# Kernel tuning notes

Measured on AMD Instinct MI355X. Metric: run time of the kernel, lower is better.

Reference implementation:

```python
import jax, jax.numpy as jnp
import numpy as np

B, NB, F, N = 8192, 64, 256, 1_000_000
K = 8            # per-channel top-k
KS = K // 2 + 1  # conv1d kernel size = 5
H, OUT = 256, 128
DN = ('NWC', 'WIO', 'NWC')


def setup_inputs() -> dict:
    key = jax.random.key(0)
    ks = jax.random.split(key, 7)
    return {
        'node_ids': jax.random.randint(ks[0], (B,), 0, N, dtype=jnp.int64) if jax.config.jax_enable_x64 else jax.random.randint(ks[0], (B,), 0, N, dtype=jnp.int32),
        'neighbors': jax.random.randint(ks[1], (B, NB), 0, N, dtype=jnp.int32),
        'feat_table': jax.random.normal(ks[2], (N, F), dtype=jnp.float32),
        'W1': jax.random.normal(ks[3], (KS, F, H), dtype=jnp.float32) * 0.05,
        'b1': jnp.zeros((H,), dtype=jnp.float32),
        'W2': jax.random.normal(ks[4], (KS, H, OUT), dtype=jnp.float32) * 0.05,
        'b2': jnp.zeros((OUT,), dtype=jnp.float32),
    }


def reference(node_ids, neighbors, feat_table, W1, b1, W2, b2):
    node_feats = feat_table[node_ids][:, None, :]          # [B, 1, F]
    nb_feats = feat_table[neighbors]                       # [B, NB, F] irregular gather
    # per-channel top-k over neighbors
    topk, _ = jax.lax.top_k(jnp.transpose(nb_feats, (0, 2, 1)), K)  # [B, F, K]
    topk = jnp.transpose(topk, (0, 2, 1))                  # [B, K, F]
    x = jnp.concatenate([node_feats, topk], axis=1)        # [B, K+1, F]
    h = jax.lax.conv_general_dilated(x, W1, (1,), 'VALID', dimension_numbers=DN) + b1  # [B, K+2-KS, H]
    o = jax.lax.conv_general_dilated(h, W2, (1,), 'VALID', dimension_numbers=DN) + b2  # [B, 1, OUT]
    return o[:, 0, :]                                      # [B, OUT]
```

## Files before the change

kernel.cpp:

```cpp
#include <hip/hip_runtime.h>
#include <hip/hip_bf16.h>

namespace {
constexpr int kB    = 8192;
constexpr int kNB   = 64;
constexpr int kF    = 256;
constexpr int kK    = 8;
constexpr int kKS   = 5;
constexpr int kH    = 256;
constexpr int kOUT  = 128;
constexpr int kXR   = 9;
constexpr int kTO   = 5;

constexpr size_t X_OFF   = 0;
constexpr size_t W1T_OFF = (size_t)kB * kXR * kF * 2;
constexpr size_t W2T_OFF = W1T_OFF + (size_t)kKS * kH * kF * 2;

typedef __attribute__((ext_vector_type(8))) short short8;
typedef __attribute__((ext_vector_type(4))) float f32x4;
}

using bf16 = __hip_bfloat16;

__device__ __forceinline__ unsigned short f2bf(float f) {
  bf16 h = __float2bfloat16(f);
  return *reinterpret_cast<unsigned short*>(&h);
}

__global__ void convert_weights(const float* __restrict__ W1,
                                const float* __restrict__ W2,
                                bf16* __restrict__ w1t, bf16* __restrict__ w2t)
{
  const int i = blockIdx.x * 256 + threadIdx.x;
  const int stride = gridDim.x * 256;
  for (int idx = i; idx < kKS * kH * kF; idx += stride) {
    const int f  = idx & 255;
    const int hc = (idx >> 8) & 255;
    const int dt = idx >> 16;
    w1t[idx] = __float2bfloat16(W1[(dt * kF + f) * kH + hc]);
  }
  for (int idx = i; idx < kOUT * kKS * kH; idx += stride) {
    const int k = idx % (kKS * kH);
    const int o = idx / (kKS * kH);
    w2t[idx] = __float2bfloat16(W2[k * kOUT + o]);
  }
}

__global__ __launch_bounds__(256)
void gather_topk(const int* __restrict__ node_ids,
                 const int* __restrict__ neighbors,
                 const float* __restrict__ feat,
                 bf16* __restrict__ x)
{
  const int wave = threadIdx.x >> 6;
  const int lane = threadIdx.x & 63;
  const int b    = blockIdx.x * 4 + wave;
  const int f4   = lane << 2;

  const int myn = neighbors[(size_t)b * kNB + lane];
  const int nid = node_ids[b];

  const float4 nodev =
      *reinterpret_cast<const float4*>(feat + (size_t)nid * kF + f4);

  float tk[4][kK];
#pragma unroll
  for (int c = 0; c < 4; ++c)
#pragma unroll
    for (int k = 0; k < kK; ++k) tk[c][k] = -INFINITY;

#pragma unroll 16
  for (int n = 0; n < kNB; ++n) {
    const int r = __builtin_amdgcn_readlane(myn, n);
    const float4 v =
        *reinterpret_cast<const float4*>(feat + (size_t)r * kF + f4);
    const float vv[4] = {v.x, v.y, v.z, v.w};
#pragma unroll
    for (int c = 0; c < 4; ++c) {
      tk[c][kK - 1] = fmaxf(tk[c][kK - 1], vv[c]);
#pragma unroll
      for (int k = kK - 1; k > 0; --k) {
        const float hi = fmaxf(tk[c][k - 1], tk[c][k]);
        const float lo = fminf(tk[c][k - 1], tk[c][k]);
        tk[c][k - 1] = hi;
        tk[c][k]     = lo;
      }
    }
  }

  bf16* xb = x + (size_t)b * kXR * kF + f4;
  {
    ushort4 s = {f2bf(nodev.x), f2bf(nodev.y), f2bf(nodev.z), f2bf(nodev.w)};
    *reinterpret_cast<ushort4*>(xb) = s;
  }
#pragma unroll
  for (int k = 0; k < kK; ++k) {
    ushort4 s = {f2bf(tk[0][k]), f2bf(tk[1][k]), f2bf(tk[2][k]), f2bf(tk[3][k])};
    *reinterpret_cast<ushort4*>(xb + (size_t)(1 + k) * kF) = s;
  }
}

__global__ __launch_bounds__(256)
void conv_gemm(const bf16* __restrict__ x, const bf16* __restrict__ w1t,
               const bf16* __restrict__ w2t, const float* __restrict__ b1,
               const float* __restrict__ b2, float* __restrict__ out)
{
  constexpr int BM   = 16;
  constexpr int XPAD = 264;
  constexpr int HPAD = 1288;

  __shared__ bf16 smem[BM * kXR * XPAD];
  bf16* xs = smem;
  bf16* hs = smem;

  const int tid  = threadIdx.x;
  const int wave = tid >> 6;
  const int lane = tid & 63;
  const int r = lane & 15;
  const int q = lane >> 4;
  const int bbase = blockIdx.x * BM;

  {
    const bf16* gx = x + (size_t)bbase * kXR * kF;
    for (int c = tid; c < BM * kXR * (kF / 8); c += 256) {
      const int f8  = c & 31;
      const int row = (c >> 5) % kXR;
      const int bb  = c / (32 * kXR);
      short8 v = *reinterpret_cast<const short8*>(gx + (size_t)c * 8);
      *reinterpret_cast<short8*>(&xs[(bb * kXR + row) * XPAD + f8 * 8]) = v;
    }
  }
  __syncthreads();

  const int ntb = wave * 64;
  f32x4 acc[kTO][4];
#pragma unroll
  for (int n = 0; n < 4; ++n) {
    const float bv = b1[ntb + n * 16 + r];
#pragma unroll
    for (int m = 0; m < kTO; ++m) acc[m][n] = (f32x4){bv, bv, bv, bv};
  }

  for (int kk = 0; kk < 8; ++kk) {
    short8 a[kXR];
#pragma unroll
    for (int rr = 0; rr < kXR; ++rr)
      a[rr] = *reinterpret_cast<const short8*>(&xs[(r * kXR + rr) * XPAD + kk * 32 + q * 8]);
#pragma unroll
    for (int dt = 0; dt < kKS; ++dt) {
      short8 bfr[4];
#pragma unroll
      for (int n = 0; n < 4; ++n)
        bfr[n] = *reinterpret_cast<const short8*>(
            &w1t[((size_t)(dt * kH + ntb + n * 16 + r)) * kF + kk * 32 + q * 8]);
#pragma unroll
      for (int m = 0; m < kTO; ++m)
#pragma unroll
        for (int n = 0; n < 4; ++n)
          acc[m][n] = __builtin_amdgcn_mfma_f32_16x16x32_bf16(a[m + dt], bfr[n], acc[m][n], 0, 0, 0);
    }
  }
  __syncthreads();

#pragma unroll
  for (int m = 0; m < kTO; ++m)
#pragma unroll
    for (int n = 0; n < 4; ++n)
#pragma unroll
      for (int j = 0; j < 4; ++j)
        hs[(q * 4 + j) * HPAD + m * kH + ntb + n * 16 + r] = __float2bfloat16(acc[m][n][j]);
  __syncthreads();

  const int ob = wave * 32;
  f32x4 acc2[2];
#pragma unroll
  for (int n = 0; n < 2; ++n) {
    const float bv = b2[ob + n * 16 + r];
    acc2[n] = (f32x4){bv, bv, bv, bv};
  }
  for (int ks = 0; ks < 40; ++ks) {
    short8 a2 = *reinterpret_cast<const short8*>(&hs[r * HPAD + ks * 32 + q * 8]);
#pragma unroll
    for (int n = 0; n < 2; ++n) {
      short8 b2f = *reinterpret_cast<const short8*>(
          &w2t[(size_t)(ob + n * 16 + r) * (kKS * kH) + ks * 32 + q * 8]);
      acc2[n] = __builtin_amdgcn_mfma_f32_16x16x32_bf16(a2, b2f, acc2[n], 0, 0, 0);
    }
  }
#pragma unroll
  for (int n = 0; n < 2; ++n)
#pragma unroll
    for (int j = 0; j < 4; ++j)
      out[(size_t)(bbase + q * 4 + j) * kOUT + ob + n * 16 + r] = acc2[n][j];
}

extern "C" void kernel_launch(void* const* d_in, const int* in_sizes, int n_in,
                              void* d_out, int out_size, void* d_ws, size_t ws_size,
                              hipStream_t stream) {
  const int*   node_ids  = (const int*)  d_in[0];
  const int*   neighbors = (const int*)  d_in[1];
  const float* feat      = (const float*)d_in[2];
  const float* W1        = (const float*)d_in[3];
  const float* b1        = (const float*)d_in[4];
  const float* W2        = (const float*)d_in[5];
  const float* b2        = (const float*)d_in[6];
  float* out = (float*)d_out;

  char* ws = (char*)d_ws;
  bf16* x_ws  = (bf16*)(ws + X_OFF);
  bf16* w1t   = (bf16*)(ws + W1T_OFF);
  bf16* w2t   = (bf16*)(ws + W2T_OFF);

  convert_weights<<<512, 256, 0, stream>>>(W1, W2, w1t, w2t);
  gather_topk<<<kB / 4, 256, 0, stream>>>(node_ids, neighbors, feat, x_ws);
  conv_gemm<<<kB / 16, 256, 0, stream>>>(x_ws, w1t, w2t, b1, b2, out);
}
```

Before: 168.6 us.

## Fuse neighbor gather and top-k into conv GEMM kernel with prefetch buffering

Merges the gather/top-k kernel into the conv GEMM kernel. Each wave computes top-k for four batch rows and writes the bf16 rows straight into LDS instead of a global workspace, which removes the intermediate x round trip and one launch. The neighbor row loads are now software-pipelined through an 8-deep register buffer to hide gather latency. The LDS padding changes to 258/1290 elements, which breaks 16-byte alignment of the vector LDS accesses, and each block now serializes gather work before its MFMA phase.

```diff
diff --git a/kernel.cpp b/kernel.cpp
--- a/kernel.cpp
+++ b/kernel.cpp
@@ -11,9 +11,12 @@
 constexpr int kOUT  = 128;
 constexpr int kXR   = 9;
 constexpr int kTO   = 5;
-
-constexpr size_t X_OFF   = 0;
-constexpr size_t W1T_OFF = (size_t)kB * kXR * kF * 2;
+constexpr int kBM   = 16;
+
+constexpr int XPAD = 258;
+constexpr int HPAD = 1290;
+
+constexpr size_t W1T_OFF = 0;
 constexpr size_t W2T_OFF = W1T_OFF + (size_t)kKS * kH * kF * 2;
 
 typedef __attribute__((ext_vector_type(8))) short short8;
@@ -47,69 +50,14 @@
 }
 
 __global__ __launch_bounds__(256)
-void gather_topk(const int* __restrict__ node_ids,
-                 const int* __restrict__ neighbors,
-                 const float* __restrict__ feat,
-                 bf16* __restrict__ x)
+void fused_all(const int* __restrict__ node_ids,
+               const int* __restrict__ neighbors,
+               const float* __restrict__ feat,
+               const bf16* __restrict__ w1t, const bf16* __restrict__ w2t,
+               const float* __restrict__ b1, const float* __restrict__ b2,
+               float* __restrict__ out)
 {
-  const int wave = threadIdx.x >> 6;
-  const int lane = threadIdx.x & 63;
-  const int b    = blockIdx.x * 4 + wave;
-  const int f4   = lane << 2;
-
-  const int myn = neighbors[(size_t)b * kNB + lane];
-  const int nid = node_ids[b];
-
-  const float4 nodev =
-      *reinterpret_cast<const float4*>(feat + (size_t)nid * kF + f4);
-
-  float tk[4][kK];
-#pragma unroll
-  for (int c = 0; c < 4; ++c)
-#pragma unroll
-    for (int k = 0; k < kK; ++k) tk[c][k] = -INFINITY;
-
-#pragma unroll 16
-  for (int n = 0; n < kNB; ++n) {
-    const int r = __builtin_amdgcn_readlane(myn, n);
-    const float4 v =
-        *reinterpret_cast<const float4*>(feat + (size_t)r * kF + f4);
-    const float vv[4] = {v.x, v.y, v.z, v.w};
-#pragma unroll
-    for (int c = 0; c < 4; ++c) {
-      tk[c][kK - 1] = fmaxf(tk[c][kK - 1], vv[c]);
-#pragma unroll
-      for (int k = kK - 1; k > 0; --k) {
-        const float hi = fmaxf(tk[c][k - 1], tk[c][k]);
-        const float lo = fminf(tk[c][k - 1], tk[c][k]);
-        tk[c][k - 1] = hi;
-        tk[c][k]     = lo;
-      }
-    }
-  }
-
-  bf16* xb = x + (size_t)b * kXR * kF + f4;
-  {
-    ushort4 s = {f2bf(nodev.x), f2bf(nodev.y), f2bf(nodev.z), f2bf(nodev.w)};
-    *reinterpret_cast<ushort4*>(xb) = s;
-  }
-#pragma unroll
-  for (int k = 0; k < kK; ++k) {
-    ushort4 s = {f2bf(tk[0][k]), f2bf(tk[1][k]), f2bf(tk[2][k]), f2bf(tk[3][k])};
-    *reinterpret_cast<ushort4*>(xb + (size_t)(1 + k) * kF) = s;
-  }
-}
-
-__global__ __launch_bounds__(256)
-void conv_gemm(const bf16* __restrict__ x, const bf16* __restrict__ w1t,
-               const bf16* __restrict__ w2t, const float* __restrict__ b1,
-               const float* __restrict__ b2, float* __restrict__ out)
-{
-  constexpr int BM   = 16;
-  constexpr int XPAD = 264;
-  constexpr int HPAD = 1288;
-
-  __shared__ bf16 smem[BM * kXR * XPAD];
+  __shared__ bf16 smem[kBM * kXR * XPAD];
   bf16* xs = smem;
   bf16* hs = smem;
 
@@ -118,16 +66,64 @@
   const int lane = tid & 63;
   const int r = lane & 15;
   const int q = lane >> 4;
-  const int bbase = blockIdx.x * BM;
-
-  {
-    const bf16* gx = x + (size_t)bbase * kXR * kF;
-    for (int c = tid; c < BM * kXR * (kF / 8); c += 256) {
-      const int f8  = c & 31;
-      const int row = (c >> 5) % kXR;
-      const int bb  = c / (32 * kXR);
-      short8 v = *reinterpret_cast<const short8*>(gx + (size_t)c * 8);
-      *reinterpret_cast<short8*>(&xs[(bb * kXR + row) * XPAD + f8 * 8]) = v;
+  const int bbase = blockIdx.x * kBM;
+  const int f4 = lane << 2;
+
+  for (int bb = 0; bb < 4; ++bb) {
+    const int bl = wave * 4 + bb;
+    const int b  = bbase + bl;
+    const int myn = neighbors[(size_t)b * kNB + lane];
+    const int nid = node_ids[b];
+    const float4 nodev = *reinterpret_cast<const float4*>(feat + (size_t)nid * kF + f4);
+
+    float tk[4][kK];
+#pragma unroll
+    for (int c = 0; c < 4; ++c)
+#pragma unroll
+      for (int k = 0; k < kK; ++k) tk[c][k] = -INFINITY;
+
+    auto ce4 = [&](const float4& v) {
+      const float vv[4] = {v.x, v.y, v.z, v.w};
+#pragma unroll
+      for (int c = 0; c < 4; ++c) {
+        tk[c][kK - 1] = fmaxf(tk[c][kK - 1], vv[c]);
+#pragma unroll
+        for (int k = kK - 1; k > 0; --k) {
+          const float hi = fmaxf(tk[c][k - 1], tk[c][k]);
+          const float lo = fminf(tk[c][k - 1], tk[c][k]);
+          tk[c][k - 1] = hi;
+          tk[c][k]     = lo;
+        }
+      }
+    };
+
+    float4 buf[8];
+#pragma unroll
+    for (int i = 0; i < 8; ++i) {
+      const int rr = __builtin_amdgcn_readlane(myn, i);
+      buf[i] = *reinterpret_cast<const float4*>(feat + (size_t)rr * kF + f4);
+    }
+    for (int g = 1; g < 8; ++g) {
+#pragma unroll
+      for (int i = 0; i < 8; ++i) {
+        const float4 v = buf[i];
+        const int rr = __builtin_amdgcn_readlane(myn, g * 8 + i);
+        buf[i] = *reinterpret_cast<const float4*>(feat + (size_t)rr * kF + f4);
+        ce4(v);
+      }
+    }
+#pragma unroll
+    for (int i = 0; i < 8; ++i) ce4(buf[i]);
+
+    bf16* xb = xs + (size_t)bl * kXR * XPAD + f4;
+    {
+      ushort4 s = {f2bf(nodev.x), f2bf(nodev.y), f2bf(nodev.z), f2bf(nodev.w)};
+      *reinterpret_cast<ushort4*>(xb) = s;
+    }
+#pragma unroll
+    for (int k = 0; k < kK; ++k) {
+      ushort4 s = {f2bf(tk[0][k]), f2bf(tk[1][k]), f2bf(tk[2][k]), f2bf(tk[3][k])};
+      *reinterpret_cast<ushort4*>(xb + (size_t)(1 + k) * XPAD) = s;
     }
   }
   __syncthreads();
@@ -207,11 +203,9 @@
   float* out = (float*)d_out;
 
   char* ws = (char*)d_ws;
-  bf16* x_ws  = (bf16*)(ws + X_OFF);
-  bf16* w1t   = (bf16*)(ws + W1T_OFF);
-  bf16* w2t   = (bf16*)(ws + W2T_OFF);
+  bf16* w1t = (bf16*)(ws + W1T_OFF);
+  bf16* w2t = (bf16*)(ws + W2T_OFF);
 
   convert_weights<<<512, 256, 0, stream>>>(W1, W2, w1t, w2t);
-  gather_topk<<<kB / 4, 256, 0, stream>>>(node_ids, neighbors, feat, x_ws);
-  conv_gemm<<<kB / 16, 256, 0, stream>>>(x_ws, w1t, w2t, b1, b2, out);
-}
+  fused_all<<<kB / kBM, 256, 0, stream>>>(node_ids, neighbors, feat, w1t, w2t, b1, b2, out);
+}
```

Result: faster. 139.1 us (-17.5%).
